# Optimization experiments

Measured on AMD Instinct MI355X. Metric: run time of the kernel, lower is better.

## Reference

```python
import jax, jax.numpy as jnp
import numpy as np


def _axis_taps(g, size):
    # g: continuous grid coordinate; returns two neighbor indices (clamped)
    # and their linear interpolation weights, matching the HDRNet CUDA kernel:
    #   w = max(1 - |i + 0.5 - g|, 0)
    f = jnp.floor(g - 0.5)
    taps = []
    for off in (0.0, 1.0):
        idx = f + off
        w = jnp.maximum(1.0 - jnp.abs(idx + 0.5 - g), 0.0)
        i = jnp.clip(idx, 0, size - 1).astype(jnp.int32)
        taps.append((i, w))
    return taps


def bilateral_slice_apply(grid, guide, inp):
    # grid: [B, gh, gw, gd, n_out*(n_in+1)]   (has_offset=True)
    # guide: [B, H, W] in [0,1]
    # inp:  [B, H, W, n_in]
    B, gh, gw, gd, nc = grid.shape
    _, H, W, n_in = inp.shape
    n_out = nc // (n_in + 1)

    # continuous grid coords for each pixel / guide value
    gx = (jnp.arange(W, dtype=grid.dtype) + 0.5) * (gw / W)   # [W]
    gy = (jnp.arange(H, dtype=grid.dtype) + 0.5) * (gh / H)   # [H]
    gz = guide * gd                                           # [B,H,W]

    x_taps = _axis_taps(gx, gw)   # idx/w: [W]
    y_taps = _axis_taps(gy, gh)   # idx/w: [H]
    z_taps = _axis_taps(gz, gd)   # idx/w: [B,H,W]

    b = jnp.arange(B)[:, None, None]
    coeff = jnp.zeros((B, H, W, nc), dtype=grid.dtype)
    for yi, wy in y_taps:
        for xi, wx in x_taps:
            for zi, wz in z_taps:
                g = grid[b, yi[None, :, None], xi[None, None, :], zi]  # [B,H,W,nc]
                w = (wy[None, :, None] * wx[None, None, :] * wz)[..., None]
                coeff = coeff + w * g

    # per-pixel affine apply: out_o = sum_i A[o,i]*in_i + A[o,n_in]
    coeff = coeff.reshape(B, H, W, n_out, n_in + 1)
    out = jnp.einsum('bhwoc,bhwc->bhwo', coeff[..., :n_in], inp) + coeff[..., n_in]
    return out


def setup_inputs() -> dict:
    key = jax.random.key(0)
    k1, k2, k3 = jax.random.split(key, 3)
    B, gh, gw, gd = 4, 16, 16, 8
    H, W, n_in, n_out = 1024, 1024, 3, 3
    nc = n_out * (n_in + 1)  # has_offset=True -> 12
    grid = jax.random.normal(k1, (B, gh, gw, gd, nc), dtype=jnp.float32)
    guide = jax.random.uniform(k2, (B, H, W), dtype=jnp.float32)
    inp = jax.random.normal(k3, (B, H, W, n_in), dtype=jnp.float32)
    return {"grid": grid, "guide": guide, "input": inp}


def reference(grid, guide, input):
    return bilateral_slice_apply(grid, guide, input)
```

## Files before the change

### kernel.cpp

```cpp
#include <hip/hip_runtime.h>
#include <hip/hip_fp16.h>


struct __align__(16) H2x4 { __half2 x, y, z, w; };
struct __align__(8)  H2x2 { __half2 a, b; };

__global__ __launch_bounds__(256, 4) void BilateralSliceApply_kernel(
    const float* __restrict__ grid,
    const float* __restrict__ guide,
    const float* __restrict__ inp,
    float* __restrict__ out)
{
    __shared__ H2x4 lA[1024];
    __shared__ H2x4 lB[512];

    const int tx = blockIdx.x;
    const int ty = blockIdx.y;
    const int b  = blockIdx.z;
    const int t  = threadIdx.x;
    const int xl = t & 63;

    const int x0 = tx << 6;
    const int y0 = ty << 5;

    const int fy  = (ty == 0) ? -1 : ((ty - 1) >> 1);
    const int ycA = fy < 0 ? 0 : fy;
    const int ycB = (fy + 1 > 15) ? 15 : fy + 1;

    const int fx  = (xl < 32) ? (tx - 1) : tx;
    const int ix0 = fx < 0 ? 0 : fx;
    const int ix1 = (fx + 1 > 15) ? 15 : fx + 1;
    const float wx1 = ((float)(x0 + xl) + 0.5f) * 0.015625f - 0.5f - (float)fx;

    const int bbase = b << 4;
    const int g0grp = t >> 6;

    const int r0 = t >> 6;
    const int pp0 = (((b << 10) + y0 + r0) << 10) + x0 + xl;
    float  gz8[8];
    float3 in8[8];
#pragma unroll
    for (int k = 0; k < 8; ++k) {
        const int pp = pp0 + (k << 12);
        gz8[k] = guide[pp];
        in8[k] = *(const float3*)(inp + (size_t)pp * 3);
    }

#pragma unroll
    for (int q = 0; q < 4; ++q) {
        const int L  = g0grp + (q << 2);
        const int yc = L >> 3;
        const int z  = L & 7;
        const int ycell = yc ? ycB : ycA;
        const int cb = (bbase + ycell) << 4;
        const float* p0 = grid + (size_t)(((cb + ix0) << 3) + z) * 12;
        const float* p1 = grid + (size_t)(((cb + ix1) << 3) + z) * 12;
        const float4 a0 = *(const float4*)(p0 + 0);
        const float4 a1 = *(const float4*)(p0 + 4);
        const float4 a2 = *(const float4*)(p0 + 8);
        const float4 b0 = *(const float4*)(p1 + 0);
        const float4 b1 = *(const float4*)(p1 + 4);
        const float4 b2 = *(const float4*)(p1 + 8);
        const float v0  = fmaf(wx1, b0.x - a0.x, a0.x);
        const float v1  = fmaf(wx1, b0.y - a0.y, a0.y);
        const float v2  = fmaf(wx1, b0.z - a0.z, a0.z);
        const float v3  = fmaf(wx1, b0.w - a0.w, a0.w);
        const float v4  = fmaf(wx1, b1.x - a1.x, a1.x);
        const float v5  = fmaf(wx1, b1.y - a1.y, a1.y);
        const float v6  = fmaf(wx1, b1.z - a1.z, a1.z);
        const float v7  = fmaf(wx1, b1.w - a1.w, a1.w);
        const float v8  = fmaf(wx1, b2.x - a2.x, a2.x);
        const float v9  = fmaf(wx1, b2.y - a2.y, a2.y);
        const float v10 = fmaf(wx1, b2.z - a2.z, a2.z);
        const float v11 = fmaf(wx1, b2.w - a2.w, a2.w);

        H2x4 rowA;
        rowA.x = __floats2half2_rn(v0, v1);
        rowA.y = __floats2half2_rn(v2, v3);
        rowA.z = __floats2half2_rn(v4, v5);
        rowA.w = __floats2half2_rn(v6, v7);
        lA[(L << 6) + xl] = rowA;

        H2x2 rowB;
        rowB.a = __floats2half2_rn(v8, v9);
        rowB.b = __floats2half2_rn(v10, v11);
        ((H2x2*)lB)[(((z << 6) + xl) << 1) + yc] = rowB;
    }
    __syncthreads();

#pragma unroll
    for (int k = 0; k < 8; ++k) {
        const int row = r0 + (k << 2);
        const int y   = y0 + row;
        const float wy1 = ((float)y + 0.5f) * 0.015625f - 0.5f - (float)fy;
        const float wy0 = 1.0f - wy1;
        const int pp = pp0 + (k << 12);

        const float gz  = gz8[k] * 8.0f;
        const float fz  = floorf(gz - 0.5f);
        const float wz1 = gz - 0.5f - fz;
        const float wz0 = 1.0f - wz1;
        const int ifz = (int)fz;
        const int iz0 = ifz < 0 ? 0 : (ifz > 7 ? 7 : ifz);
        const int nz  = ifz + 1;
        const int iz1 = nz < 0 ? 0 : (nz > 7 ? 7 : nz);

        const __half2 hA0 = __float2half2_rn(wy0 * wz0);
        const __half2 hA1 = __float2half2_rn(wy0 * wz1);
        const __half2 hB0 = __float2half2_rn(wy1 * wz0);
        const __half2 hB1 = __float2half2_rn(wy1 * wz1);

        const H2x4 vA00 = lA[(iz0 << 6) + xl];
        const H2x4 vA01 = lA[(iz1 << 6) + xl];
        const H2x4 vA10 = lA[((8 + iz0) << 6) + xl];
        const H2x4 vA11 = lA[((8 + iz1) << 6) + xl];
        const H2x4 vB0  = lB[(iz0 << 6) + xl];
        const H2x4 vB1  = lB[(iz1 << 6) + xl];

        __half2 q0 = __hmul2(hA0, vA00.x);
        __half2 q1 = __hmul2(hA0, vA00.y);
        __half2 q2 = __hmul2(hA0, vA00.z);
        __half2 q3 = __hmul2(hA0, vA00.w);
        q0 = __hfma2(hA1, vA01.x, q0);
        q1 = __hfma2(hA1, vA01.y, q1);
        q2 = __hfma2(hA1, vA01.z, q2);
        q3 = __hfma2(hA1, vA01.w, q3);
        q0 = __hfma2(hB0, vA10.x, q0);
        q1 = __hfma2(hB0, vA10.y, q1);
        q2 = __hfma2(hB0, vA10.z, q2);
        q3 = __hfma2(hB0, vA10.w, q3);
        q0 = __hfma2(hB1, vA11.x, q0);
        q1 = __hfma2(hB1, vA11.y, q1);
        q2 = __hfma2(hB1, vA11.z, q2);
        q3 = __hfma2(hB1, vA11.w, q3);

        __half2 q4 = __hmul2(hA0, vB0.x);
        __half2 q5 = __hmul2(hA0, vB0.y);
        q4 = __hfma2(hA1, vB1.x, q4);
        q5 = __hfma2(hA1, vB1.y, q5);
        q4 = __hfma2(hB0, vB0.z, q4);
        q5 = __hfma2(hB0, vB0.w, q5);
        q4 = __hfma2(hB1, vB1.z, q4);
        q5 = __hfma2(hB1, vB1.w, q5);

        const float3 in = in8[k];
        const __half2 i01 = __floats2half2_rn(in.x, in.y);
        const __half2 i21 = __floats2half2_rn(in.z, 1.0f);

        __half2 r0h = __hmul2(q0, i01); r0h = __hfma2(q1, i21, r0h);
        __half2 r1h = __hmul2(q2, i01); r1h = __hfma2(q3, i21, r1h);
        __half2 r2h = __hmul2(q4, i01); r2h = __hfma2(q5, i21, r2h);

        float3 o;
        o.x = __low2float(r0h) + __high2float(r0h);
        o.y = __low2float(r1h) + __high2float(r1h);
        o.z = __low2float(r2h) + __high2float(r2h);
        *(float3*)(out + (size_t)pp * 3) = o;
    }
}

extern "C" void kernel_launch(void* const* d_in, const int* in_sizes, int n_in,
                              void* d_out, int out_size, void* d_ws, size_t ws_size,
                              hipStream_t stream) {
    const float* grid  = (const float*)d_in[0];
    const float* guide = (const float*)d_in[1];
    const float* inp   = (const float*)d_in[2];
    float* out = (float*)d_out;

    dim3 gridDim(16, 32, 4);
    BilateralSliceApply_kernel<<<gridDim, 256, 0, stream>>>(grid, guide, inp, out);
}
```

Before: 115.9 us.

## Process 64-row tiles per block, staging three grid rows and splitting pixel loads

Each block now covers 64 rows instead of 32, so it stages x-interpolated coefficients for three adjacent grid y-cells in shared memory, with the offset channels packed per y-pair. This halves the block count and spreads the grid-staging cost over twice as many pixels. The second half of the guide and input loads is issued after the staging barrier to overlap with work. Costs are fewer blocks in flight, more shared memory per block, and more live registers from two prefetched pixel batches.

```diff
diff --git a/kernel.cpp b/kernel.cpp
--- a/kernel.cpp
+++ b/kernel.cpp
@@ -3,7 +3,6 @@
 
 
 struct __align__(16) H2x4 { __half2 x, y, z, w; };
-struct __align__(8)  H2x2 { __half2 a, b; };
 
 __global__ __launch_bounds__(256, 4) void BilateralSliceApply_kernel(
     const float* __restrict__ grid,
@@ -11,92 +10,104 @@
     const float* __restrict__ inp,
     float* __restrict__ out)
 {
-    __shared__ H2x4 lA[1024];
-    __shared__ H2x4 lB[512];
+    __shared__ H2x4 lA[24 * 64];
+    __shared__ H2x4 lB[16 * 64];
 
     const int tx = blockIdx.x;
     const int ty = blockIdx.y;
     const int b  = blockIdx.z;
     const int t  = threadIdx.x;
     const int xl = t & 63;
+    const int r0 = t >> 6;
 
     const int x0 = tx << 6;
-    const int y0 = ty << 5;
+    const int y0 = ty << 6;
 
-    const int fy  = (ty == 0) ? -1 : ((ty - 1) >> 1);
-    const int ycA = fy < 0 ? 0 : fy;
-    const int ycB = (fy + 1 > 15) ? 15 : fy + 1;
+    const int s0 = ty > 0 ? ty - 1 : 0;
+    const int s1 = ty;
+    const int s2 = ty < 15 ? ty + 1 : 15;
+
+    const int pp0 = (((b << 10) + y0 + r0) << 10) + x0 + xl;
+    float  gzA[8];
+    float3 inA[8];
+#pragma unroll
+    for (int k = 0; k < 8; ++k) {
+        const int pp = pp0 + (k << 12);
+        gzA[k] = guide[pp];
+        inA[k] = *(const float3*)(inp + (size_t)pp * 3);
+    }
 
     const int fx  = (xl < 32) ? (tx - 1) : tx;
     const int ix0 = fx < 0 ? 0 : fx;
     const int ix1 = (fx + 1 > 15) ? 15 : fx + 1;
     const float wx1 = ((float)(x0 + xl) + 0.5f) * 0.015625f - 0.5f - (float)fx;
+    const int bbase = b << 4;
 
-    const int bbase = b << 4;
-    const int g0grp = t >> 6;
+    for (int L = r0; L < 40; L += 4) {
+        const int z = L & 7;
+        const int w = L >> 3;
+        if (w < 3) {
+            const int ycell = (w == 0) ? s0 : (w == 1 ? s1 : s2);
+            const int cb = (bbase + ycell) << 4;
+            const float* p0 = grid + (size_t)(((cb + ix0) << 3) + z) * 12;
+            const float* p1 = grid + (size_t)(((cb + ix1) << 3) + z) * 12;
+            const float4 a0 = *(const float4*)(p0 + 0);
+            const float4 a1 = *(const float4*)(p0 + 4);
+            const float4 b0 = *(const float4*)(p1 + 0);
+            const float4 b1 = *(const float4*)(p1 + 4);
+            H2x4 r;
+            r.x = __floats2half2_rn(fmaf(wx1, b0.x - a0.x, a0.x),
+                                    fmaf(wx1, b0.y - a0.y, a0.y));
+            r.y = __floats2half2_rn(fmaf(wx1, b0.z - a0.z, a0.z),
+                                    fmaf(wx1, b0.w - a0.w, a0.w));
+            r.z = __floats2half2_rn(fmaf(wx1, b1.x - a1.x, a1.x),
+                                    fmaf(wx1, b1.y - a1.y, a1.y));
+            r.w = __floats2half2_rn(fmaf(wx1, b1.z - a1.z, a1.z),
+                                    fmaf(wx1, b1.w - a1.w, a1.w));
+            lA[(L << 6) + xl] = r;
+        } else {
+            const int v  = w - 3;
+            const int pA = v ? s1 : s0;
+            const int pB = v ? s2 : s1;
+            const int cbA = (bbase + pA) << 4;
+            const int cbB = (bbase + pB) << 4;
+            const float4 a0 = *(const float4*)(grid + (size_t)(((cbA + ix0) << 3) + z) * 12 + 8);
+            const float4 a1 = *(const float4*)(grid + (size_t)(((cbA + ix1) << 3) + z) * 12 + 8);
+            const float4 b0 = *(const float4*)(grid + (size_t)(((cbB + ix0) << 3) + z) * 12 + 8);
+            const float4 b1 = *(const float4*)(grid + (size_t)(((cbB + ix1) << 3) + z) * 12 + 8);
+            H2x4 r;
+            r.x = __floats2half2_rn(fmaf(wx1, a1.x - a0.x, a0.x),
+                                    fmaf(wx1, a1.y - a0.y, a0.y));
+            r.y = __floats2half2_rn(fmaf(wx1, a1.z - a0.z, a0.z),
+                                    fmaf(wx1, a1.w - a0.w, a0.w));
+            r.z = __floats2half2_rn(fmaf(wx1, b1.x - b0.x, b0.x),
+                                    fmaf(wx1, b1.y - b0.y, b0.y));
+            r.w = __floats2half2_rn(fmaf(wx1, b1.z - b0.z, b0.z),
+                                    fmaf(wx1, b1.w - b0.w, b0.w));
+            lB[((L - 24) << 6) + xl] = r;
+        }
+    }
+    __syncthreads();
 
-    const int r0 = t >> 6;
-    const int pp0 = (((b << 10) + y0 + r0) << 10) + x0 + xl;
-    float  gz8[8];
-    float3 in8[8];
+    float  gzB[8];
+    float3 inB[8];
 #pragma unroll
     for (int k = 0; k < 8; ++k) {
-        const int pp = pp0 + (k << 12);
-        gz8[k] = guide[pp];
-        in8[k] = *(const float3*)(inp + (size_t)pp * 3);
+        const int pp = pp0 + ((k + 8) << 12);
+        gzB[k] = guide[pp];
+        inB[k] = *(const float3*)(inp + (size_t)pp * 3);
     }
 
 #pragma unroll
-    for (int q = 0; q < 4; ++q) {
-        const int L  = g0grp + (q << 2);
-        const int yc = L >> 3;
-        const int z  = L & 7;
-        const int ycell = yc ? ycB : ycA;
-        const int cb = (bbase + ycell) << 4;
-        const float* p0 = grid + (size_t)(((cb + ix0) << 3) + z) * 12;
-        const float* p1 = grid + (size_t)(((cb + ix1) << 3) + z) * 12;
-        const float4 a0 = *(const float4*)(p0 + 0);
-        const float4 a1 = *(const float4*)(p0 + 4);
-        const float4 a2 = *(const float4*)(p0 + 8);
-        const float4 b0 = *(const float4*)(p1 + 0);
-        const float4 b1 = *(const float4*)(p1 + 4);
-        const float4 b2 = *(const float4*)(p1 + 8);
-        const float v0  = fmaf(wx1, b0.x - a0.x, a0.x);
-        const float v1  = fmaf(wx1, b0.y - a0.y, a0.y);
-        const float v2  = fmaf(wx1, b0.z - a0.z, a0.z);
-        const float v3  = fmaf(wx1, b0.w - a0.w, a0.w);
-        const float v4  = fmaf(wx1, b1.x - a1.x, a1.x);
-        const float v5  = fmaf(wx1, b1.y - a1.y, a1.y);
-        const float v6  = fmaf(wx1, b1.z - a1.z, a1.z);
-        const float v7  = fmaf(wx1, b1.w - a1.w, a1.w);
-        const float v8  = fmaf(wx1, b2.x - a2.x, a2.x);
-        const float v9  = fmaf(wx1, b2.y - a2.y, a2.y);
-        const float v10 = fmaf(wx1, b2.z - a2.z, a2.z);
-        const float v11 = fmaf(wx1, b2.w - a2.w, a2.w);
+    for (int k = 0; k < 16; ++k) {
+        const int v   = k >> 3;
+        const int row = r0 + (k << 2);
+        const int pp  = pp0 + (k << 12);
 
-        H2x4 rowA;
-        rowA.x = __floats2half2_rn(v0, v1);
-        rowA.y = __floats2half2_rn(v2, v3);
-        rowA.z = __floats2half2_rn(v4, v5);
-        rowA.w = __floats2half2_rn(v6, v7);
-        lA[(L << 6) + xl] = rowA;
+        const float wy1 = ((float)row + 0.5f) * 0.015625f + (v ? -0.5f : 0.5f);
+        const float wy0 = 1.0f - wy1;
 
-        H2x2 rowB;
-        rowB.a = __floats2half2_rn(v8, v9);
-        rowB.b = __floats2half2_rn(v10, v11);
-        ((H2x2*)lB)[(((z << 6) + xl) << 1) + yc] = rowB;
-    }
-    __syncthreads();
-
-#pragma unroll
-    for (int k = 0; k < 8; ++k) {
-        const int row = r0 + (k << 2);
-        const int y   = y0 + row;
-        const float wy1 = ((float)y + 0.5f) * 0.015625f - 0.5f - (float)fy;
-        const float wy0 = 1.0f - wy1;
-        const int pp = pp0 + (k << 12);
-
-        const float gz  = gz8[k] * 8.0f;
+        const float gz  = (v ? gzB[k - 8] : gzA[k]) * 8.0f;
         const float fz  = floorf(gz - 0.5f);
         const float wz1 = gz - 0.5f - fz;
         const float wz0 = 1.0f - wz1;
@@ -110,12 +121,15 @@
         const __half2 hB0 = __float2half2_rn(wy1 * wz0);
         const __half2 hB1 = __float2half2_rn(wy1 * wz1);
 
-        const H2x4 vA00 = lA[(iz0 << 6) + xl];
-        const H2x4 vA01 = lA[(iz1 << 6) + xl];
-        const H2x4 vA10 = lA[((8 + iz0) << 6) + xl];
-        const H2x4 vA11 = lA[((8 + iz1) << 6) + xl];
-        const H2x4 vB0  = lB[(iz0 << 6) + xl];
-        const H2x4 vB1  = lB[(iz1 << 6) + xl];
+        const int slotLo = v;
+        const int slotHi = v + 1;
+
+        const H2x4 vA00 = lA[(((slotLo << 3) + iz0) << 6) + xl];
+        const H2x4 vA01 = lA[(((slotLo << 3) + iz1) << 6) + xl];
+        const H2x4 vA10 = lA[(((slotHi << 3) + iz0) << 6) + xl];
+        const H2x4 vA11 = lA[(((slotHi << 3) + iz1) << 6) + xl];
+        const H2x4 vB0  = lB[(((v << 3) + iz0) << 6) + xl];
+        const H2x4 vB1  = lB[(((v << 3) + iz1) << 6) + xl];
 
         __half2 q0 = __hmul2(hA0, vA00.x);
         __half2 q1 = __hmul2(hA0, vA00.y);
@@ -143,7 +157,7 @@
         q4 = __hfma2(hB1, vB1.z, q4);
         q5 = __hfma2(hB1, vB1.w, q5);
 
-        const float3 in = in8[k];
+        const float3 in = v ? inB[k - 8] : inA[k];
         const __half2 i01 = __floats2half2_rn(in.x, in.y);
         const __half2 i21 = __floats2half2_rn(in.z, 1.0f);
 
@@ -167,6 +181,6 @@
     const float* inp   = (const float*)d_in[2];
     float* out = (float*)d_out;
 
-    dim3 gridDim(16, 32, 4);
+    dim3 gridDim(16, 16, 4);
     BilateralSliceApply_kernel<<<gridDim, 256, 0, stream>>>(grid, guide, inp, out);
 }
```

New measurement: 117.0 us. About the same (+1.0%).
